# Kernel tuning notes

Measured on AMD Instinct MI355X. Metric: run time of the kernel, lower is better.

The kernel has to match this reference:

```python
import jax, jax.numpy as jnp
import numpy as np
from jax import lax

DIM = 64
HID = int(DIM * 2.67)  # 170, matches torch int(dim*ffn_expansion_factor)
EPS_LN = 1e-5
EPS_NORM = 1e-12


def _conv1x1(x, w, b):
    # x: [B,C,H,W], w: [O,C], b: [O]
    return jnp.einsum('oc,bchw->bohw', w, x) + b[None, :, None, None]


def _dwconv3(x, w, b):
    # depthwise 3x3, w: [C,1,3,3]
    y = lax.conv_general_dilated(x, w, (1, 1), 'SAME',
                                 dimension_numbers=('NCHW', 'OIHW', 'NCHW'),
                                 feature_group_count=x.shape[1])
    return y + b[None, :, None, None]


def _ln_channel(x, w, b):
    # WithBias LayerNorm over channel dim (torch does to_3d then LN over c)
    mu = jnp.mean(x, axis=1, keepdims=True)
    var = jnp.mean((x - mu) ** 2, axis=1, keepdims=True)
    return (x - mu) / jnp.sqrt(var + EPS_LN) * w[None, :, None, None] + b[None, :, None, None]


def _l2norm(x):
    n = jnp.sqrt(jnp.sum(x * x, axis=-1, keepdims=True))
    return x / jnp.maximum(n, EPS_NORM)


def _attn_wxw(x, ln_w, ln_b, qkv_w, qkv_b, dw_w, dw_b, pw, pb, temp):
    m = x
    y = _ln_channel(x, ln_w, ln_b)
    qkv = _dwconv3(_conv1x1(y, qkv_w, qkv_b), dw_w, dw_b)
    q, k, v = jnp.split(qkv, 3, axis=1)
    B, C, H, W = q.shape
    q2 = _l2norm(q.reshape(B, C * H, W))  # 'b c h w -> b (c h) w', normalize over w
    k2 = _l2norm(k.reshape(B, C * H, W))
    attn = jax.nn.softmax(jnp.einsum('bnw,bnu->bwu', q2, k2) * temp[0, 0], axis=-1)  # [B,W,W]
    out = jnp.einsum('bchw,bwu->bchu', v, attn)  # v @ attn with broadcast head dim
    return _conv1x1(out, pw, pb) + m


def _attn_hxh(x, ln_w, ln_b, qkv_w, qkv_b, dw_w, dw_b, pw, pb, temp):
    m = x
    y = _ln_channel(x, ln_w, ln_b)
    qkv = _dwconv3(_conv1x1(y, qkv_w, qkv_b), dw_w, dw_b)
    q, k, v = jnp.split(qkv, 3, axis=1)
    B, C, H, W = q.shape
    q2 = _l2norm(jnp.transpose(q, (0, 2, 1, 3)).reshape(B, H, C * W))  # 'b c h w -> b h (c w)'
    k2 = _l2norm(jnp.transpose(k, (0, 2, 1, 3)).reshape(B, H, C * W))
    attn = jax.nn.softmax(jnp.einsum('bhn,bgn->bhg', q2, k2) * temp[0, 0], axis=-1)  # [B,H,H]
    out = jnp.einsum('bhg,bcgw->bchw', attn, v)  # attn @ v with broadcast head dim
    return _conv1x1(out, pw, pb) + m


def _ffn(x, in_w, in_b, dw_w, dw_b, out_w, out_b):
    y = _dwconv3(_conv1x1(x, in_w, in_b), dw_w, dw_b)
    x1, x2 = jnp.split(y, 2, axis=1)
    return _conv1x1(jax.nn.gelu(x1, approximate=False) * x2, out_w, out_b)


def setup_inputs() -> dict:
    key = jax.random.key(0)
    ks = iter(jax.random.split(key, 32))
    B, C, H, W = 4, DIM, 256, 256
    s = 0.02

    def nrm(shape):
        return jax.random.normal(next(ks), shape, dtype=jnp.float32) * s

    d = {
        'x': jax.random.normal(next(ks), (B, C, H, W), dtype=jnp.float32),
        'zero_map': jnp.ones((B, 1, H, W), dtype=jnp.float32),
    }
    for p in ('w', 'h'):
        d[p + '_ln_w'] = jnp.ones((C,), jnp.float32)
        d[p + '_ln_b'] = jnp.zeros((C,), jnp.float32)
        d[p + '_qkv_w'] = nrm((3 * C, C))
        d[p + '_qkv_b'] = jnp.zeros((3 * C,), jnp.float32)
        d[p + '_dw_w'] = nrm((3 * C, 1, 3, 3))
        d[p + '_dw_b'] = jnp.zeros((3 * C,), jnp.float32)
        d[p + '_proj_w'] = nrm((C, C))
        d[p + '_proj_b'] = jnp.zeros((C,), jnp.float32)
        d[p + '_temp'] = jnp.ones((1, 1), jnp.float32)
    d['n2_w'] = jnp.ones((C,), jnp.float32)
    d['n2_b'] = jnp.zeros((C,), jnp.float32)
    d['ffn_in_w'] = nrm((2 * HID, C))
    d['ffn_in_b'] = jnp.zeros((2 * HID,), jnp.float32)
    d['ffn_dw_w'] = nrm((2 * HID, 1, 3, 3))
    d['ffn_dw_b'] = jnp.zeros((2 * HID,), jnp.float32)
    d['ffn_out_w'] = nrm((C, HID))
    d['ffn_out_b'] = jnp.zeros((C,), jnp.float32)
    return d


def reference(x, zero_map,
              w_ln_w, w_ln_b, w_qkv_w, w_qkv_b, w_dw_w, w_dw_b, w_proj_w, w_proj_b, w_temp,
              h_ln_w, h_ln_b, h_qkv_w, h_qkv_b, h_dw_w, h_dw_b, h_proj_w, h_proj_b, h_temp,
              n2_w, n2_b,
              ffn_in_w, ffn_in_b, ffn_dw_w, ffn_dw_b, ffn_out_w, ffn_out_b):
    # DeepTransformerBlock_withnoZeromap.forward (zero_map is unused in the torch code)
    m = _attn_wxw(x, w_ln_w, w_ln_b, w_qkv_w, w_qkv_b, w_dw_w, w_dw_b, w_proj_w, w_proj_b, w_temp)
    z = _attn_hxh(m, h_ln_w, h_ln_b, h_qkv_w, h_qkv_b, h_dw_w, h_dw_b, h_proj_w, h_proj_b, h_temp)
    return z + _ffn(_ln_channel(z, n2_w, n2_b), ffn_in_w, ffn_in_b, ffn_dw_w, ffn_dw_b, ffn_out_w, ffn_out_b)
```

## Files before the change

kernel.cpp:

```cpp
#include <hip/hip_runtime.h>
#include <math.h>
#include <stdint.h>

#define P_ 65536

#define DW_OFF   0ul
#define QKV_OFF  12582912ul
#define ATTP_OFF QKV_OFF
#define Y_OFF    25165824ul
#define ATT_OFF  31457280ul
#define HID_OFF  0ul
#define G_OFF    22282240ul
#define WSB      33423360ul

typedef unsigned short ush;
typedef __attribute__((ext_vector_type(8))) short bf16x8;
typedef __attribute__((ext_vector_type(4))) float f32x4;

__device__ __forceinline__ ush f2bf(float f) {
    uint32_t u = __float_as_uint(f);
    return (ush)((u + 0x7FFFu + ((u >> 16) & 1u)) >> 16);
}
__device__ __forceinline__ float bf2f(ush h) {
    return __uint_as_float((uint32_t)h << 16);
}

template<int CIN, int CPAD, int COUT, int COPAD, int PX, bool LN, bool RES,
         bool INBF, bool OUTBF>
__global__ __launch_bounds__(256) void conv_mfma_kernel(
        const void* __restrict__ in_, const float* __restrict__ lnw,
        const float* __restrict__ lnb, const float* __restrict__ Wt,
        const float* __restrict__ bias, void* __restrict__ out_,
        const float* __restrict__ res_, size_t zi, size_t zo, size_t zr) {
    static_assert(!(RES && OUTBF), "res only with fp32 out");
    constexpr int NSL = CPAD / 32;
    constexpr int NMT = PX / 16;
    constexpr bool HOIST = (CPAD == 64 && PX == 128);
    __shared__ ush sX[PX * CPAD];
    __shared__ ush sW[COPAD * CPAD];
    __shared__ float sPa[LN ? 256 : 1], sPb[LN ? 256 : 1];
    __shared__ float sMu[LN ? 128 : 1], sInv[LN ? 128 : 1];
    int tid = threadIdx.x;
    int hw0 = blockIdx.x * PX;
    int obase = blockIdx.y * COPAD;
    int lane = tid & 63, wave = tid >> 6;

    {
        uint32_t* sX32 = (uint32_t*)sX;
        #pragma unroll
        for (int it = 0; it < PX * CPAD / 512; ++it) {
            int idx = tid + it * 256;
            int p = idx & (PX - 1), c = (idx / PX) * 2;
            uint32_t pk;
            if constexpr (INBF) {
                const ush* in = (const ush*)in_ + (size_t)blockIdx.z * zi;
                ush a = (c < CIN)     ? in[(size_t)c * P_ + hw0 + p]     : (ush)0;
                ush b = (c + 1 < CIN) ? in[(size_t)(c+1) * P_ + hw0 + p] : (ush)0;
                pk = (uint32_t)a | ((uint32_t)b << 16);
            } else {
                const float* in = (const float*)in_ + (size_t)blockIdx.z * zi;
                float v0 = (c < CIN)     ? in[(size_t)c * P_ + hw0 + p]     : 0.f;
                float v1 = (c + 1 < CIN) ? in[(size_t)(c+1) * P_ + hw0 + p] : 0.f;
                pk = (uint32_t)f2bf(v0) | ((uint32_t)f2bf(v1) << 16);
            }
            int kb = c >> 3;
            sX32[(p * CPAD + (((kb ^ (p & 7)) << 3) | (c & 7))) >> 1] = pk;
        }
    }
    {
        uint32_t* sW32 = (uint32_t*)sW;
        #pragma unroll
        for (int it = 0; it < COPAD * CPAD / 512; ++it) {
            int idx = tid + it * 256;
            int c2 = idx % (CPAD / 2), o = idx / (CPAD / 2);
            int c = c2 * 2, og = obase + o;
            float v0 = (og < COUT && c < CIN)     ? Wt[(size_t)og * CIN + c]     : 0.f;
            float v1 = (og < COUT && c + 1 < CIN) ? Wt[(size_t)og * CIN + c + 1] : 0.f;
            uint32_t pk = (uint32_t)f2bf(v0) | ((uint32_t)f2bf(v1) << 16);
            int kb = c >> 3;
            sW32[(o * CPAD + (((kb ^ (o & 7)) << 3) | (c & 7))) >> 1] = pk;
        }
    }
    __syncthreads();
    if constexpr (LN) {
        static_assert(!LN || (CPAD == 64 && PX == 128), "LN path assumes 64ch/128px");
        int p = tid & 127, q = tid >> 7;
        float s = 0.f, s2 = 0.f;
        #pragma unroll
        for (int c = q * 32; c < q * 32 + 32; ++c) {
            float v = bf2f(sX[p * 64 + ((((c >> 3) ^ (p & 7)) << 3) | (c & 7))]);
            s += v; s2 += v * v;
        }
        sPa[tid] = s; sPb[tid] = s2;
        __syncthreads();
        if (tid < 128) {
            float ss = sPa[tid] + sPa[tid+128];
            float qq = sPb[tid] + sPb[tid+128];
            float mu = ss * (1.f/64.f);
            float var = qq * (1.f/64.f) - mu * mu;
            sMu[tid] = mu; sInv[tid] = rsqrtf(var + 1e-5f);
        }
        __syncthreads();
        float mu = sMu[p], inv = sInv[p];
        #pragma unroll
        for (int c = q * 32; c < q * 32 + 32; ++c) {
            int sw = p * 64 + ((((c >> 3) ^ (p & 7)) << 3) | (c & 7));
            float v = bf2f(sX[sw]);
            sX[sw] = f2bf((v - mu) * inv * lnw[c] + lnb[c]);
        }
        __syncthreads();
    }

    int pxl = lane & 15, quad = lane >> 4;
    int olim = (COUT - obase < COPAD) ? (COUT - obase) : COPAD;
    int ntile = (olim + 15) >> 4;
    bf16x8 xf[HOIST ? NMT * NSL : 1];
    if constexpr (HOIST) {
        #pragma unroll
        for (int m = 0; m < NMT; ++m)
            #pragma unroll
            for (int s = 0; s < NSL; ++s) {
                int p = m * 16 + pxl;
                int kb = s * 4 + quad;
                xf[m * NSL + s] = *(const bf16x8*)&sX[p * CPAD + ((kb ^ (p & 7)) << 3)];
            }
    }
    for (int ot = wave; ot < ntile; ot += 4) {
        int on = ot * 16 + pxl;
        int og = obase + on;
        f32x4 acc[NMT];
        #pragma unroll
        for (int m = 0; m < NMT; ++m) acc[m] = (f32x4){0.f, 0.f, 0.f, 0.f};
        #pragma unroll
        for (int s = 0; s < NSL; ++s) {
            int kb = s * 4 + quad;
            bf16x8 wf = *(const bf16x8*)&sW[on * CPAD + ((kb ^ (on & 7)) << 3)];
            #pragma unroll
            for (int m = 0; m < NMT; ++m) {
                bf16x8 af;
                if constexpr (HOIST) af = xf[m * NSL + s];
                else {
                    int p = m * 16 + pxl;
                    af = *(const bf16x8*)&sX[p * CPAD + ((kb ^ (p & 7)) << 3)];
                }
                acc[m] = __builtin_amdgcn_mfma_f32_16x16x32_bf16(af, wf, acc[m], 0, 0, 0);
            }
        }
        bool oval = og < COUT;
        float bv = oval ? bias[og] : 0.f;
        #pragma unroll
        for (int m = 0; m < NMT; ++m) {
            if (oval) {
                size_t ob = (size_t)og * P_ + hw0 + m * 16 + quad * 4;
                if constexpr (OUTBF) {
                    ush* out = (ush*)out_ + (size_t)blockIdx.z * zo;
                    ushort4 sv;
                    sv.x = f2bf(acc[m][0] + bv); sv.y = f2bf(acc[m][1] + bv);
                    sv.z = f2bf(acc[m][2] + bv); sv.w = f2bf(acc[m][3] + bv);
                    *(ushort4*)&out[ob] = sv;
                } else {
                    float* out = (float*)out_ + (size_t)blockIdx.z * zo;
                    float4 v = make_float4(acc[m][0] + bv, acc[m][1] + bv,
                                           acc[m][2] + bv, acc[m][3] + bv);
                    if constexpr (RES) {
                        const float* res = res_ + (size_t)blockIdx.z * zr;
                        float4 rv = *(const float4*)&res[ob];
                        v.x += rv.x; v.y += rv.y; v.z += rv.z; v.w += rv.w;
                    }
                    *(float4*)&out[ob] = v;
                }
            }
        }
    }
}

__device__ __forceinline__ void mfma_step64(const ush* sA,
        const ush* sB, int wave, int lane, f32x4 acc[2][8]) {
    int pxl = lane & 15, quad = lane >> 4;
    #pragma unroll
    for (int s = 0; s < 2; ++s) {
        int kb = s * 4 + quad;
        bf16x8 af[2];
        #pragma unroll
        for (int mt = 0; mt < 2; ++mt) {
            int im = wave * 32 + mt * 16 + pxl;
            af[mt] = *(const bf16x8*)&sA[im * 64 + ((kb ^ (im & 7)) << 3)];
        }
        #pragma unroll
        for (int jt = 0; jt < 8; ++jt) {
            int jn = jt * 16 + pxl;
            bf16x8 bf = *(const bf16x8*)&sB[jn * 64 + ((kb ^ (jn & 7)) << 3)];
            #pragma unroll
            for (int mt = 0; mt < 2; ++mt)
                acc[mt][jt] = __builtin_amdgcn_mfma_f32_16x16x32_bf16(af[mt], bf, acc[mt][jt], 0, 0, 0);
        }
    }
}

#define STAGE_DIRECT64(sDst, ROWADDR, Q)                                     \
    {   uint32_t* s32_ = (uint32_t*)(sDst);                                  \
        _Pragma("unroll")                                                    \
        for (int it_ = 0; it_ < 8; ++it_) {                                  \
            int idx_ = tid + it_ * 256;                                      \
            int il_ = idx_ >> 4, k_ = (idx_ & 15) * 4;                       \
            float4 v_ = *(const float4*)(ROWADDR(il_) + (Q) * 64 + k_);      \
            uint32_t p0_ = (uint32_t)f2bf(v_.x) | ((uint32_t)f2bf(v_.y) << 16); \
            uint32_t p1_ = (uint32_t)f2bf(v_.z) | ((uint32_t)f2bf(v_.w) << 16); \
            int off_ = il_ * 64 + ((((k_ >> 3) ^ (il_ & 7)) << 3) | (k_ & 7)); \
            s32_[off_ >> 1] = p0_;                                           \
            s32_[(off_ >> 1) + 1] = p1_;                                     \
        }                                                                    \
    }

#define STAGE_TRANS64(sDst, KROWADDR, Q)                                     \
    {   _Pragma("unroll")                                                    \
        for (int it_ = 0; it_ < 8; ++it_) {                                  \
            int idx_ = tid + it_ * 256;                                      \
            int r_ = idx_ >> 5, il4_ = (idx_ & 31) * 4;                      \
            float4 v_ = *(const float4*)(KROWADDR((Q) * 64 + r_) + il4_);    \
            float vv_[4] = {v_.x, v_.y, v_.z, v_.w};                         \
            int kb_ = r_ >> 3;                                               \
            _Pragma("unroll")                                                \
            for (int e_ = 0; e_ < 4; ++e_) {                                 \
                int il_ = il4_ + e_;                                         \
                (sDst)[il_ * 64 + (((kb_ ^ (il_ & 7)) << 3) | (r_ & 7))] = f2bf(vv_[e_]); \
            }                                                                \
        }                                                                    \
    }

#define STAGE_DIRECT64_BF(sDst, ROWADDR, Q)                                  \
    {   _Pragma("unroll")                                                    \
        for (int it_ = 0; it_ < 8; ++it_) {                                  \
            int idx_ = tid + it_ * 256;                                      \
            int il_ = idx_ >> 4, k_ = (idx_ & 15) * 4;                       \
            ushort4 v_ = *(const ushort4*)(ROWADDR(il_) + (Q) * 64 + k_);    \
            int off_ = il_ * 64 + ((((k_ >> 3) ^ (il_ & 7)) << 3) | (k_ & 7)); \
            *(ushort4*)&(sDst)[off_] = v_;                                   \
        }                                                                    \
    }

#define STAGE_TRANS64_BF(sDst, KROWADDR, Q)                                  \
    {   _Pragma("unroll")                                                    \
        for (int it_ = 0; it_ < 8; ++it_) {                                  \
            int idx_ = tid + it_ * 256;                                      \
            int r_ = idx_ >> 5, il4_ = (idx_ & 31) * 4;                      \
            ushort4 v_ = *(const ushort4*)(KROWADDR((Q) * 64 + r_) + il4_);  \
            ush vv_[4] = {v_.x, v_.y, v_.z, v_.w};                          \
            int kb_ = r_ >> 3;                                               \
            _Pragma("unroll")                                                \
            for (int e_ = 0; e_ < 4; ++e_) {                                 \
                int il_ = il4_ + e_;                                         \
                (sDst)[il_ * 64 + (((kb_ ^ (il_ & 7)) << 3) | (r_ & 7))] = vv_[e_]; \
            }                                                                \
        }                                                                    \
    }

template<bool HXH>
__global__ __launch_bounds__(256) void attn_logits_mfma(const ush* __restrict__ dw_,
        float* __restrict__ part_, size_t zd, size_t zp) {
    __shared__ ush sA[128 * 64];
    __shared__ ush sB[128 * 64];
    const ush* dw = dw_ + (size_t)blockIdx.z * zd;
    float* part = part_ + (size_t)blockIdx.z * zp;
    int tid = threadIdx.x, lane = tid & 63, wave = tid >> 6;
    int i0 = (blockIdx.x & 1) * 128, j0 = (blockIdx.x >> 1) * 128;
    int ks = blockIdx.y;
    const ush* qc = dw + ((size_t)ks << 16);
    const ush* kc = dw + ((size_t)(64 + ks) << 16);
    f32x4 acc[2][8];
    #pragma unroll
    for (int mt = 0; mt < 2; ++mt)
        #pragma unroll
        for (int jt = 0; jt < 8; ++jt) acc[mt][jt] = (f32x4){0.f, 0.f, 0.f, 0.f};
    for (int q = 0; q < 4; ++q) {
        if (q) __syncthreads();
        if constexpr (HXH) {
            #define ROWA_Q(il) (qc + (size_t)(i0 + (il)) * 256)
            #define ROWA_K(il) (kc + (size_t)(j0 + (il)) * 256)
            STAGE_DIRECT64_BF(sA, ROWA_Q, q)
            STAGE_DIRECT64_BF(sB, ROWA_K, q)
            #undef ROWA_Q
            #undef ROWA_K
        } else {
            #define KROW_Q(r) (qc + (size_t)(r) * 256 + i0)
            #define KROW_K(r) (kc + (size_t)(r) * 256 + j0)
            STAGE_TRANS64_BF(sA, KROW_Q, q)
            STAGE_TRANS64_BF(sB, KROW_K, q)
            #undef KROW_Q
            #undef KROW_K
        }
        __syncthreads();
        mfma_step64(sA, sB, wave, lane, acc);
    }
    int pxl = lane & 15, quad = lane >> 4;
    float* pb = part + ((size_t)ks << 16);
    #pragma unroll
    for (int mt = 0; mt < 2; ++mt) {
        #pragma unroll
        for (int jt = 0; jt < 8; ++jt) {
            #pragma unroll
            for (int r = 0; r < 4; ++r) {
                int i = i0 + wave * 32 + mt * 16 + quad * 4 + r;
                int j = j0 + jt * 16 + pxl;
                pb[(size_t)i * 256 + j] = acc[mt][jt][r];
            }
        }
    }
}

__global__ __launch_bounds__(256) void av_w_mfma(const ush* __restrict__ dw_,
        const float* __restrict__ att_, ush* __restrict__ out_,
        size_t zd, size_t za, size_t zo) {
    __shared__ ush sA[128 * 64];
    __shared__ ush sB[128 * 64];
    const ush* dw = dw_ + (size_t)blockIdx.z * zd;
    const float* att = att_ + (size_t)blockIdx.z * za;
    ush* out = out_ + (size_t)blockIdx.z * zo;
    int tid = threadIdx.x, lane = tid & 63, wave = tid >> 6;
    int m0 = blockIdx.x * 128, u0 = blockIdx.y * 128;
    f32x4 acc[2][8];
    #pragma unroll
    for (int mt = 0; mt < 2; ++mt)
        #pragma unroll
        for (int jt = 0; jt < 8; ++jt) acc[mt][jt] = (f32x4){0.f, 0.f, 0.f, 0.f};
    for (int q = 0; q < 4; ++q) {
        if (q) __syncthreads();
        #define ROWA_V(il) (dw + ((size_t)(128 + ((m0 + (il)) & 63)) << 16) \
                               + ((m0 + (il)) >> 6) * 256)
        #define KROW_ATT(r) (att + (size_t)(r) * 256 + u0)
        STAGE_DIRECT64_BF(sA, ROWA_V, q)
        STAGE_TRANS64(sB, KROW_ATT, q)
        #undef ROWA_V
        #undef KROW_ATT
        __syncthreads();
        mfma_step64(sA, sB, wave, lane, acc);
    }
    int pxl = lane & 15, quad = lane >> 4;
    #pragma unroll
    for (int mt = 0; mt < 2; ++mt) {
        #pragma unroll
        for (int jt = 0; jt < 8; ++jt) {
            #pragma unroll
            for (int r = 0; r < 4; ++r) {
                int m = m0 + wave * 32 + mt * 16 + quad * 4 + r;
                int c = m & 63, h = m >> 6;
                out[((size_t)c << 16) + h * 256 + u0 + jt * 16 + pxl] = f2bf(acc[mt][jt][r]);
            }
        }
    }
}

__global__ __launch_bounds__(256) void av_h_mfma(const ush* __restrict__ dw_,
        const float* __restrict__ att_, ush* __restrict__ out_,
        size_t zd, size_t za, size_t zo) {
    __shared__ ush sA[128 * 64];
    __shared__ ush sB[128 * 64];
    const ush* dw = dw_ + (size_t)blockIdx.z * zd;
    const float* att = att_ + (size_t)blockIdx.z * za;
    ush* out = out_ + (size_t)blockIdx.z * zo;
    int tid = threadIdx.x, lane = tid & 63, wave = tid >> 6;
    int c = blockIdx.x >> 1;
    int w0 = (blockIdx.x & 1) * 128;
    int h0 = blockIdx.y * 128;
    const ush* vc = dw + ((size_t)(128 + c) << 16);
    f32x4 acc[2][8];
    #pragma unroll
    for (int mt = 0; mt < 2; ++mt)
        #pragma unroll
        for (int jt = 0; jt < 8; ++jt) acc[mt][jt] = (f32x4){0.f, 0.f, 0.f, 0.f};
    for (int q = 0; q < 4; ++q) {
        if (q) __syncthreads();
        #define ROWA_ATT(il) (att + (size_t)(h0 + (il)) * 256)
        #define KROW_V(r) (vc + (size_t)(r) * 256 + w0)
        STAGE_DIRECT64(sA, ROWA_ATT, q)
        STAGE_TRANS64_BF(sB, KROW_V, q)
        #undef ROWA_ATT
        #undef KROW_V
        __syncthreads();
        mfma_step64(sA, sB, wave, lane, acc);
    }
    int pxl = lane & 15, quad = lane >> 4;
    #pragma unroll
    for (int mt = 0; mt < 2; ++mt) {
        #pragma unroll
        for (int jt = 0; jt < 8; ++jt) {
            #pragma unroll
            for (int r = 0; r < 4; ++r) {
                int h = h0 + wave * 32 + mt * 16 + quad * 4 + r;
                out[((size_t)c << 16) + h * 256 + w0 + jt * 16 + pxl] = f2bf(acc[mt][jt][r]);
            }
        }
    }
}

__global__ __launch_bounds__(256) void softmax_kernel(const float* __restrict__ part_,
        const float* __restrict__ temp, float* __restrict__ att_,
        size_t zp, size_t za) {
    const float* part = part_ + (size_t)blockIdx.z * zp;
    float* att = att_ + (size_t)blockIdx.z * za;
    int i = blockIdx.x;
    int j = threadIdx.x;
    size_t rowoff = (size_t)i * 256 + j;
    float s = 0.f;
    #pragma unroll
    for (int kk = 0; kk < 64; ++kk) s += part[(size_t)kk * 65536 + rowoff];
    s *= temp[0];
    __shared__ float redA[4], redB[4];
    int wv = j >> 6, ln = j & 63;
    float m = s;
    #pragma unroll
    for (int off = 32; off; off >>= 1) m = fmaxf(m, __shfl_down(m, off, 64));
    if (ln == 0) redA[wv] = m;
    __syncthreads();
    m = fmaxf(fmaxf(redA[0], redA[1]), fmaxf(redA[2], redA[3]));
    float e = expf(s - m);
    float t2 = e;
    #pragma unroll
    for (int off = 32; off; off >>= 1) t2 += __shfl_down(t2, off, 64);
    if (ln == 0) redB[wv] = t2;
    __syncthreads();
    float tot = redB[0] + redB[1] + redB[2] + redB[3];
    att[rowoff] = e / tot;
}

template<bool NORM>
__global__ __launch_bounds__(256) void dw_row_kernel(const ush* __restrict__ in_,
        const float* __restrict__ w9, const float* __restrict__ bias,
        ush* __restrict__ out_, size_t zi, size_t zo) {
    const ush* in = in_ + (size_t)blockIdx.z * zi;
    ush* out = out_ + (size_t)blockIdx.z * zo;
    int row = __builtin_amdgcn_readfirstlane(blockIdx.x * 4 + (threadIdx.x >> 6));
    int o = row >> 8, h = row & 255;
    int lane = threadIdx.x & 63;
    const ush* ip = in + ((size_t)o << 16);
    const float* wp = w9 + o * 9;
    float b = bias[o];
    float4 acc = make_float4(b, b, b, b);
    #pragma unroll
    for (int dy = -1; dy <= 1; ++dy) {
        int hh = h + dy;
        float4 v = make_float4(0.f, 0.f, 0.f, 0.f);
        if (hh >= 0 && hh <= 255) {
            ushort4 t = *(const ushort4*)(ip + hh * 256 + lane * 4);
            v = make_float4(bf2f(t.x), bf2f(t.y), bf2f(t.z), bf2f(t.w));
        }
        float lft = __shfl(v.w, lane - 1);
        float rgt = __shfl(v.x, lane + 1);
        if (lane == 0)  lft = 0.f;
        if (lane == 63) rgt = 0.f;
        float w0 = wp[(dy+1)*3], w1 = wp[(dy+1)*3+1], w2 = wp[(dy+1)*3+2];
        acc.x += w0*lft + w1*v.x + w2*v.y;
        acc.y += w0*v.x + w1*v.y + w2*v.z;
        acc.z += w0*v.y + w1*v.z + w2*v.w;
        acc.w += w0*v.z + w1*v.w + w2*rgt;
    }
    if constexpr (NORM) {
        if (o < 128) {
            float s = acc.x*acc.x + acc.y*acc.y + acc.z*acc.z + acc.w*acc.w;
            #pragma unroll
            for (int off = 32; off; off >>= 1) s += __shfl_xor(s, off, 64);
            float inv = 1.0f / fmaxf(sqrtf(s), 1e-12f);
            acc.x *= inv; acc.y *= inv; acc.z *= inv; acc.w *= inv;
        }
    }
    ushort4 s4;
    s4.x = f2bf(acc.x); s4.y = f2bf(acc.y); s4.z = f2bf(acc.z); s4.w = f2bf(acc.w);
    *(ushort4*)(out + ((size_t)o << 16) + h * 256 + lane * 4) = s4;
}

__global__ __launch_bounds__(256) void ffn_dw_row_kernel(const ush* __restrict__ hid_,
        const float* __restrict__ w9, const float* __restrict__ bias,
        ush* __restrict__ g_, size_t zi, size_t zo) {
    const ush* hid = hid_ + (size_t)blockIdx.z * zi;
    ush* g = g_ + (size_t)blockIdx.z * zo;
    int row = __builtin_amdgcn_readfirstlane(blockIdx.x * 4 + (threadIdx.x >> 6));
    int i = row >> 8, h = row & 255;
    int lane = threadIdx.x & 63;
    const ush* ip1 = hid + ((size_t)i << 16);
    const ush* ip2 = ip1 + ((size_t)170 << 16);
    const float* wp1 = w9 + i * 9;
    const float* wp2 = w9 + (i + 170) * 9;
    float ba = bias[i], bb = bias[i + 170];
    float4 a = make_float4(ba, ba, ba, ba);
    float4 c = make_float4(bb, bb, bb, bb);
    #pragma unroll
    for (int dy = -1; dy <= 1; ++dy) {
        int hh = h + dy;
        float4 v1 = make_float4(0.f, 0.f, 0.f, 0.f);
        float4 v2 = make_float4(0.f, 0.f, 0.f, 0.f);
        if (hh >= 0 && hh <= 255) {
            ushort4 t1 = *(const ushort4*)(ip1 + hh * 256 + lane * 4);
            ushort4 t2 = *(const ushort4*)(ip2 + hh * 256 + lane * 4);
            v1 = make_float4(bf2f(t1.x), bf2f(t1.y), bf2f(t1.z), bf2f(t1.w));
            v2 = make_float4(bf2f(t2.x), bf2f(t2.y), bf2f(t2.z), bf2f(t2.w));
        }
        float l1 = __shfl(v1.w, lane - 1), r1 = __shfl(v1.x, lane + 1);
        float l2 = __shfl(v2.w, lane - 1), r2 = __shfl(v2.x, lane + 1);
        if (lane == 0)  { l1 = 0.f; l2 = 0.f; }
        if (lane == 63) { r1 = 0.f; r2 = 0.f; }
        float u0 = wp1[(dy+1)*3], u1 = wp1[(dy+1)*3+1], u2 = wp1[(dy+1)*3+2];
        float q0 = wp2[(dy+1)*3], q1 = wp2[(dy+1)*3+1], q2 = wp2[(dy+1)*3+2];
        a.x += u0*l1   + u1*v1.x + u2*v1.y;
        a.y += u0*v1.x + u1*v1.y + u2*v1.z;
        a.z += u0*v1.y + u1*v1.z + u2*v1.w;
        a.w += u0*v1.z + u1*v1.w + u2*r1;
        c.x += q0*l2   + q1*v2.x + q2*v2.y;
        c.y += q0*v2.x + q1*v2.y + q2*v2.z;
        c.z += q0*v2.y + q1*v2.z + q2*v2.w;
        c.w += q0*v2.z + q1*v2.w + q2*r2;
    }
    const float ISQ2 = 0.70710678118654752440f;
    ushort4 s4;
    s4.x = f2bf(0.5f * a.x * (1.0f + erff(a.x * ISQ2)) * c.x);
    s4.y = f2bf(0.5f * a.y * (1.0f + erff(a.y * ISQ2)) * c.y);
    s4.z = f2bf(0.5f * a.z * (1.0f + erff(a.z * ISQ2)) * c.z);
    s4.w = f2bf(0.5f * a.w * (1.0f + erff(a.w * ISQ2)) * c.w);
    *(ushort4*)(g + ((size_t)i << 16) + h * 256 + lane * 4) = s4;
}

__global__ __launch_bounds__(256) void l2norm_h_kernel(ush* __restrict__ dw_,
        size_t zd) {
    ush* dw = dw_ + (size_t)blockIdx.z * zd;
    int h = blockIdx.x, qk = blockIdx.y;
    ush* base = dw + ((size_t)(qk*64) << 16) + h*256;
    int tid = threadIdx.x;
    float s = 0.f;
    for (int idx = tid; idx < 4096; idx += 256) {
        int c = idx >> 6, w4 = (idx & 63) * 4;
        ushort4 t = *(const ushort4*)&base[((size_t)c << 16) + w4];
        float a = bf2f(t.x), b = bf2f(t.y), cc = bf2f(t.z), d = bf2f(t.w);
        s += a*a + b*b + cc*cc + d*d;
    }
    #pragma unroll
    for (int off = 32; off; off >>= 1) s += __shfl_down(s, off, 64);
    __shared__ float red[4];
    int wv = tid >> 6, ln = tid & 63;
    if (ln == 0) red[wv] = s;
    __syncthreads();
    float tot = red[0] + red[1] + red[2] + red[3];
    float inv = 1.0f / fmaxf(sqrtf(tot), 1e-12f);
    for (int idx = tid; idx < 4096; idx += 256) {
        int c = idx >> 6, w4 = (idx & 63) * 4;
        ushort4 t = *(const ushort4*)&base[((size_t)c << 16) + w4];
        ushort4 o;
        o.x = f2bf(bf2f(t.x) * inv); o.y = f2bf(bf2f(t.y) * inv);
        o.z = f2bf(bf2f(t.z) * inv); o.w = f2bf(bf2f(t.w) * inv);
        *(ushort4*)&base[((size_t)c << 16) + w4] = o;
    }
}

extern "C" void kernel_launch(void* const* d_in, const int* in_sizes, int n_in,
                              void* d_out, int out_size, void* d_ws, size_t ws_size,
                              hipStream_t stream) {
    (void)in_sizes; (void)n_in; (void)out_size;
    const float* x = (const float*)d_in[0];
    float* ws  = (float*)d_ws;
    float* out = (float*)d_out;
    const size_t XB = (size_t)64 * P_;
    const size_t WSB2 = 2 * WSB;
    const size_t SLAB_BYTES = WSB * sizeof(float);
    int nb = 1;
    if (ws_size >= 4 * SLAB_BYTES) nb = 4;
    else if (ws_size >= 2 * SLAB_BYTES) nb = 2;

    for (int b0 = 0; b0 < 4; b0 += nb) {
        int zc = (4 - b0 < nb) ? (4 - b0) : nb;
        const float* xb = x + (size_t)b0 * XB;
        float* outb = out + (size_t)b0 * XB;
        ush*   DW   = (ush*)(ws + DW_OFF);
        ush*   QKV  = (ush*)(ws + QKV_OFF);
        float* ATTP = ws + ATTP_OFF;
        ush*   Y    = (ush*)(ws + Y_OFF);
        float* ATT  = ws + ATT_OFF;
        ush*   HID  = (ush*)(ws + HID_OFF);
        ush*   G    = (ush*)(ws + G_OFF);

        conv_mfma_kernel<64,64,192,128,128,true,false,false,true>
            <<<dim3(512,2,zc), 256, 0, stream>>>(
                xb, (const float*)d_in[2], (const float*)d_in[3],
                (const float*)d_in[4], (const float*)d_in[5], QKV, nullptr,
                XB, WSB2, 0);
        dw_row_kernel<true><<<dim3(12288,1,zc), 256, 0, stream>>>(QKV,
                (const float*)d_in[6], (const float*)d_in[7], DW, WSB2, WSB2);
        attn_logits_mfma<false><<<dim3(4,64,zc), 256, 0, stream>>>(DW, ATTP, WSB2, WSB);
        softmax_kernel<<<dim3(256,1,zc), 256, 0, stream>>>(ATTP,
                (const float*)d_in[10], ATT, WSB, WSB);
        av_w_mfma<<<dim3(128,2,zc), 256, 0, stream>>>(DW, ATT, Y, WSB2, WSB, WSB2);
        conv_mfma_kernel<64,64,64,64,128,false,true,true,false>
            <<<dim3(512,1,zc), 256, 0, stream>>>(
                Y, nullptr, nullptr,
                (const float*)d_in[8], (const float*)d_in[9], outb, xb,
                WSB2, XB, XB);

        conv_mfma_kernel<64,64,192,128,128,true,false,false,true>
            <<<dim3(512,2,zc), 256, 0, stream>>>(
                outb, (const float*)d_in[11], (const float*)d_in[12],
                (const float*)d_in[13], (const float*)d_in[14], QKV, nullptr,
                XB, WSB2, 0);
        dw_row_kernel<false><<<dim3(12288,1,zc), 256, 0, stream>>>(QKV,
                (const float*)d_in[15], (const float*)d_in[16], DW, WSB2, WSB2);
        l2norm_h_kernel<<<dim3(256,2,zc), 256, 0, stream>>>(DW, WSB2);
        attn_logits_mfma<true><<<dim3(4,64,zc), 256, 0, stream>>>(DW, ATTP, WSB2, WSB);
        softmax_kernel<<<dim3(256,1,zc), 256, 0, stream>>>(ATTP,
                (const float*)d_in[19], ATT, WSB, WSB);
        av_h_mfma<<<dim3(128,2,zc), 256, 0, stream>>>(DW, ATT, Y, WSB2, WSB, WSB2);
        conv_mfma_kernel<64,64,64,64,128,false,true,true,false>
            <<<dim3(512,1,zc), 256, 0, stream>>>(
                Y, nullptr, nullptr,
                (const float*)d_in[17], (const float*)d_in[18], outb, outb,
                WSB2, XB, XB);

        conv_mfma_kernel<64,64,340,128,128,true,false,false,true>
            <<<dim3(512,3,zc), 256, 0, stream>>>(
                outb, (const float*)d_in[20], (const float*)d_in[21],
                (const float*)d_in[22], (const float*)d_in[23], HID, nullptr,
                XB, WSB2, 0);
        ffn_dw_row_kernel<<<dim3(10880,1,zc), 256, 0, stream>>>(HID,
                (const float*)d_in[24], (const float*)d_in[25], G, WSB2, WSB2);
        conv_mfma_kernel<170,192,64,64,64,false,true,true,false>
            <<<dim3(1024,1,zc), 256, 0, stream>>>(
                G, nullptr, nullptr,
                (const float*)d_in[26], (const float*)d_in[27], outb, outb,
                WSB2, XB, XB);
    }
}
```

Baseline: 1.158 ms.

## Fold LayerNorm into conv epilogue, halve logits partials, two rows per dwconv wave

The LayerNorm-fused 1x1 conv no longer normalizes the staged input tile in shared memory. It folds the LN weight into the conv weights and applies mean, inverse std and a precomputed bias correction per output channel in the epilogue. The attention-logits kernel now accumulates two channel slices per block, which halves the partial buffers the softmax must sum. The depthwise conv kernels compute two output rows per wave so neighbouring input rows are loaded once. The LN fold changes where bf16 rounding happens and adds a serial per-channel dot product of length CIN in every block.

```diff
diff --git a/kernel.cpp b/kernel.cpp
--- a/kernel.cpp
+++ b/kernel.cpp
@@ -33,6 +33,7 @@
         const float* __restrict__ bias, void* __restrict__ out_,
         const float* __restrict__ res_, size_t zi, size_t zo, size_t zr) {
     static_assert(!(RES && OUTBF), "res only with fp32 out");
+    static_assert(!LN || (CPAD == 64 && PX == 128), "LN path assumes 64ch/128px");
     constexpr int NSL = CPAD / 32;
     constexpr int NMT = PX / 16;
     constexpr bool HOIST = (CPAD == 64 && PX == 128);
@@ -40,6 +41,7 @@
     __shared__ ush sW[COPAD * CPAD];
     __shared__ float sPa[LN ? 256 : 1], sPb[LN ? 256 : 1];
     __shared__ float sMu[LN ? 128 : 1], sInv[LN ? 128 : 1];
+    __shared__ float sR[LN ? COPAD : 1], sK[LN ? COPAD : 1];
     int tid = threadIdx.x;
     int hw0 = blockIdx.x * PX;
     int obase = blockIdx.y * COPAD;
@@ -76,6 +78,10 @@
             int c = c2 * 2, og = obase + o;
             float v0 = (og < COUT && c < CIN)     ? Wt[(size_t)og * CIN + c]     : 0.f;
             float v1 = (og < COUT && c + 1 < CIN) ? Wt[(size_t)og * CIN + c + 1] : 0.f;
+            if constexpr (LN) {
+                if (og < COUT && c < CIN)     v0 *= lnw[c];
+                if (og < COUT && c + 1 < CIN) v1 *= lnw[c + 1];
+            }
             uint32_t pk = (uint32_t)f2bf(v0) | ((uint32_t)f2bf(v1) << 16);
             int kb = c >> 3;
             sW32[(o * CPAD + (((kb ^ (o & 7)) << 3) | (c & 7))) >> 1] = pk;
@@ -83,7 +89,6 @@
     }
     __syncthreads();
     if constexpr (LN) {
-        static_assert(!LN || (CPAD == 64 && PX == 128), "LN path assumes 64ch/128px");
         int p = tid & 127, q = tid >> 7;
         float s = 0.f, s2 = 0.f;
         #pragma unroll
@@ -92,6 +97,18 @@
             s += v; s2 += v * v;
         }
         sPa[tid] = s; sPb[tid] = s2;
+        if (tid < COPAD) {
+            int og = obase + tid;
+            float r = 0.f, k = 0.f;
+            if (og < COUT) {
+                #pragma unroll 8
+                for (int c = 0; c < CIN; ++c) {
+                    float w = Wt[(size_t)og * CIN + c];
+                    r += w * lnw[c]; k += w * lnb[c];
+                }
+            }
+            sR[tid] = r; sK[tid] = k;
+        }
         __syncthreads();
         if (tid < 128) {
             float ss = sPa[tid] + sPa[tid+128];
@@ -99,14 +116,6 @@
             float mu = ss * (1.f/64.f);
             float var = qq * (1.f/64.f) - mu * mu;
             sMu[tid] = mu; sInv[tid] = rsqrtf(var + 1e-5f);
-        }
-        __syncthreads();
-        float mu = sMu[p], inv = sInv[p];
-        #pragma unroll
-        for (int c = q * 32; c < q * 32 + 32; ++c) {
-            int sw = p * 64 + ((((c >> 3) ^ (p & 7)) << 3) | (c & 7));
-            float v = bf2f(sX[sw]);
-            sX[sw] = f2bf((v - mu) * inv * lnw[c] + lnb[c]);
         }
         __syncthreads();
     }
@@ -148,20 +157,33 @@
         }
         bool oval = og < COUT;
         float bv = oval ? bias[og] : 0.f;
+        float Rv = 0.f, Kv = 0.f;
+        if constexpr (LN) { Rv = oval ? sR[on] : 0.f; Kv = oval ? sK[on] : 0.f; }
         #pragma unroll
         for (int m = 0; m < NMT; ++m) {
             if (oval) {
                 size_t ob = (size_t)og * P_ + hw0 + m * 16 + quad * 4;
+                float o0, o1, o2, o3;
+                if constexpr (LN) {
+                    int pl = m * 16 + quad * 4;
+                    float4 mu = *(float4*)&sMu[pl];
+                    float4 iv = *(float4*)&sInv[pl];
+                    o0 = iv.x * (acc[m][0] - mu.x * Rv) + Kv + bv;
+                    o1 = iv.y * (acc[m][1] - mu.y * Rv) + Kv + bv;
+                    o2 = iv.z * (acc[m][2] - mu.z * Rv) + Kv + bv;
+                    o3 = iv.w * (acc[m][3] - mu.w * Rv) + Kv + bv;
+                } else {
+                    o0 = acc[m][0] + bv; o1 = acc[m][1] + bv;
+                    o2 = acc[m][2] + bv; o3 = acc[m][3] + bv;
+                }
                 if constexpr (OUTBF) {
                     ush* out = (ush*)out_ + (size_t)blockIdx.z * zo;
                     ushort4 sv;
-                    sv.x = f2bf(acc[m][0] + bv); sv.y = f2bf(acc[m][1] + bv);
-                    sv.z = f2bf(acc[m][2] + bv); sv.w = f2bf(acc[m][3] + bv);
+                    sv.x = f2bf(o0); sv.y = f2bf(o1); sv.z = f2bf(o2); sv.w = f2bf(o3);
                     *(ushort4*)&out[ob] = sv;
                 } else {
                     float* out = (float*)out_ + (size_t)blockIdx.z * zo;
-                    float4 v = make_float4(acc[m][0] + bv, acc[m][1] + bv,
-                                           acc[m][2] + bv, acc[m][3] + bv);
+                    float4 v = make_float4(o0, o1, o2, o3);
                     if constexpr (RES) {
                         const float* res = res_ + (size_t)blockIdx.z * zr;
                         float4 rv = *(const float4*)&res[ob];
@@ -264,36 +286,39 @@
     float* part = part_ + (size_t)blockIdx.z * zp;
     int tid = threadIdx.x, lane = tid & 63, wave = tid >> 6;
     int i0 = (blockIdx.x & 1) * 128, j0 = (blockIdx.x >> 1) * 128;
-    int ks = blockIdx.y;
-    const ush* qc = dw + ((size_t)ks << 16);
-    const ush* kc = dw + ((size_t)(64 + ks) << 16);
+    int ks2 = blockIdx.y;
     f32x4 acc[2][8];
     #pragma unroll
     for (int mt = 0; mt < 2; ++mt)
         #pragma unroll
         for (int jt = 0; jt < 8; ++jt) acc[mt][jt] = (f32x4){0.f, 0.f, 0.f, 0.f};
-    for (int q = 0; q < 4; ++q) {
-        if (q) __syncthreads();
-        if constexpr (HXH) {
-            #define ROWA_Q(il) (qc + (size_t)(i0 + (il)) * 256)
-            #define ROWA_K(il) (kc + (size_t)(j0 + (il)) * 256)
-            STAGE_DIRECT64_BF(sA, ROWA_Q, q)
-            STAGE_DIRECT64_BF(sB, ROWA_K, q)
-            #undef ROWA_Q
-            #undef ROWA_K
-        } else {
-            #define KROW_Q(r) (qc + (size_t)(r) * 256 + i0)
-            #define KROW_K(r) (kc + (size_t)(r) * 256 + j0)
-            STAGE_TRANS64_BF(sA, KROW_Q, q)
-            STAGE_TRANS64_BF(sB, KROW_K, q)
-            #undef KROW_Q
-            #undef KROW_K
-        }
-        __syncthreads();
-        mfma_step64(sA, sB, wave, lane, acc);
+    for (int cc = 0; cc < 2; ++cc) {
+        int ks = ks2 * 2 + cc;
+        const ush* qc = dw + ((size_t)ks << 16);
+        const ush* kc = dw + ((size_t)(64 + ks) << 16);
+        for (int q = 0; q < 4; ++q) {
+            if (cc | q) __syncthreads();
+            if constexpr (HXH) {
+                #define ROWA_Q(il) (qc + (size_t)(i0 + (il)) * 256)
+                #define ROWA_K(il) (kc + (size_t)(j0 + (il)) * 256)
+                STAGE_DIRECT64_BF(sA, ROWA_Q, q)
+                STAGE_DIRECT64_BF(sB, ROWA_K, q)
+                #undef ROWA_Q
+                #undef ROWA_K
+            } else {
+                #define KROW_Q(r) (qc + (size_t)(r) * 256 + i0)
+                #define KROW_K(r) (kc + (size_t)(r) * 256 + j0)
+                STAGE_TRANS64_BF(sA, KROW_Q, q)
+                STAGE_TRANS64_BF(sB, KROW_K, q)
+                #undef KROW_Q
+                #undef KROW_K
+            }
+            __syncthreads();
+            mfma_step64(sA, sB, wave, lane, acc);
+        }
     }
     int pxl = lane & 15, quad = lane >> 4;
-    float* pb = part + ((size_t)ks << 16);
+    float* pb = part + ((size_t)ks2 << 16);
     #pragma unroll
     for (int mt = 0; mt < 2; ++mt) {
         #pragma unroll
@@ -403,7 +428,7 @@
     size_t rowoff = (size_t)i * 256 + j;
     float s = 0.f;
     #pragma unroll
-    for (int kk = 0; kk < 64; ++kk) s += part[(size_t)kk * 65536 + rowoff];
+    for (int kk = 0; kk < 32; ++kk) s += part[(size_t)kk * 65536 + rowoff];
     s *= temp[0];
     __shared__ float redA[4], redB[4];
     int wv = j >> 6, ln = j & 63;
@@ -429,43 +454,63 @@
         ush* __restrict__ out_, size_t zi, size_t zo) {
     const ush* in = in_ + (size_t)blockIdx.z * zi;
     ush* out = out_ + (size_t)blockIdx.z * zo;
-    int row = __builtin_amdgcn_readfirstlane(blockIdx.x * 4 + (threadIdx.x >> 6));
-    int o = row >> 8, h = row & 255;
+    int pr = __builtin_amdgcn_readfirstlane(blockIdx.x * 4 + (threadIdx.x >> 6));
+    int o = pr >> 7, h0 = (pr & 127) * 2;
     int lane = threadIdx.x & 63;
     const ush* ip = in + ((size_t)o << 16);
     const float* wp = w9 + o * 9;
     float b = bias[o];
-    float4 acc = make_float4(b, b, b, b);
-    #pragma unroll
-    for (int dy = -1; dy <= 1; ++dy) {
-        int hh = h + dy;
-        float4 v = make_float4(0.f, 0.f, 0.f, 0.f);
+    float4 r[4];
+    float lft[4], rgt[4];
+    #pragma unroll
+    for (int k = 0; k < 4; ++k) {
+        int hh = h0 - 1 + k;
+        r[k] = make_float4(0.f, 0.f, 0.f, 0.f);
         if (hh >= 0 && hh <= 255) {
             ushort4 t = *(const ushort4*)(ip + hh * 256 + lane * 4);
-            v = make_float4(bf2f(t.x), bf2f(t.y), bf2f(t.z), bf2f(t.w));
-        }
-        float lft = __shfl(v.w, lane - 1);
-        float rgt = __shfl(v.x, lane + 1);
-        if (lane == 0)  lft = 0.f;
-        if (lane == 63) rgt = 0.f;
-        float w0 = wp[(dy+1)*3], w1 = wp[(dy+1)*3+1], w2 = wp[(dy+1)*3+2];
-        acc.x += w0*lft + w1*v.x + w2*v.y;
-        acc.y += w0*v.x + w1*v.y + w2*v.z;
-        acc.z += w0*v.y + w1*v.z + w2*v.w;
-        acc.w += w0*v.z + w1*v.w + w2*rgt;
+            r[k] = make_float4(bf2f(t.x), bf2f(t.y), bf2f(t.z), bf2f(t.w));
+        }
+        lft[k] = __shfl(r[k].w, lane - 1);
+        rgt[k] = __shfl(r[k].x, lane + 1);
+        if (lane == 0)  lft[k] = 0.f;
+        if (lane == 63) rgt[k] = 0.f;
+    }
+    float4 a0 = make_float4(b, b, b, b), a1 = a0;
+    #pragma unroll
+    for (int dy = 0; dy < 3; ++dy) {
+        float w0 = wp[dy*3], w1 = wp[dy*3+1], w2 = wp[dy*3+2];
+        float4 v = r[dy]; float l = lft[dy], rr = rgt[dy];
+        a0.x += w0*l   + w1*v.x + w2*v.y;
+        a0.y += w0*v.x + w1*v.y + w2*v.z;
+        a0.z += w0*v.y + w1*v.z + w2*v.w;
+        a0.w += w0*v.z + w1*v.w + w2*rr;
+        v = r[dy+1]; l = lft[dy+1]; rr = rgt[dy+1];
+        a1.x += w0*l   + w1*v.x + w2*v.y;
+        a1.y += w0*v.x + w1*v.y + w2*v.z;
+        a1.z += w0*v.y + w1*v.z + w2*v.w;
+        a1.w += w0*v.z + w1*v.w + w2*rr;
     }
     if constexpr (NORM) {
         if (o < 128) {
-            float s = acc.x*acc.x + acc.y*acc.y + acc.z*acc.z + acc.w*acc.w;
+            float s0 = a0.x*a0.x + a0.y*a0.y + a0.z*a0.z + a0.w*a0.w;
+            float s1 = a1.x*a1.x + a1.y*a1.y + a1.z*a1.z + a1.w*a1.w;
             #pragma unroll
-            for (int off = 32; off; off >>= 1) s += __shfl_xor(s, off, 64);
-            float inv = 1.0f / fmaxf(sqrtf(s), 1e-12f);
-            acc.x *= inv; acc.y *= inv; acc.z *= inv; acc.w *= inv;
+            for (int off = 32; off; off >>= 1) {
+                s0 += __shfl_xor(s0, off, 64);
+                s1 += __shfl_xor(s1, off, 64);
+            }
+            float i0 = 1.0f / fmaxf(sqrtf(s0), 1e-12f);
+            float i1 = 1.0f / fmaxf(sqrtf(s1), 1e-12f);
+            a0.x *= i0; a0.y *= i0; a0.z *= i0; a0.w *= i0;
+            a1.x *= i1; a1.y *= i1; a1.z *= i1; a1.w *= i1;
         }
     }
     ushort4 s4;
-    s4.x = f2bf(acc.x); s4.y = f2bf(acc.y); s4.z = f2bf(acc.z); s4.w = f2bf(acc.w);
-    *(ushort4*)(out + ((size_t)o << 16) + h * 256 + lane * 4) = s4;
+    ush* ob = out + ((size_t)o << 16) + h0 * 256 + lane * 4;
+    s4.x = f2bf(a0.x); s4.y = f2bf(a0.y); s4.z = f2bf(a0.z); s4.w = f2bf(a0.w);
+    *(ushort4*)ob = s4;
+    s4.x = f2bf(a1.x); s4.y = f2bf(a1.y); s4.z = f2bf(a1.z); s4.w = f2bf(a1.w);
+    *(ushort4*)(ob + 256) = s4;
 }
 
 __global__ __launch_bounds__(256) void ffn_dw_row_kernel(const ush* __restrict__ hid_,
@@ -473,49 +518,72 @@
         ush* __restrict__ g_, size_t zi, size_t zo) {
     const ush* hid = hid_ + (size_t)blockIdx.z * zi;
     ush* g = g_ + (size_t)blockIdx.z * zo;
-    int row = __builtin_amdgcn_readfirstlane(blockIdx.x * 4 + (threadIdx.x >> 6));
-    int i = row >> 8, h = row & 255;
+    int pr = __builtin_amdgcn_readfirstlane(blockIdx.x * 4 + (threadIdx.x >> 6));
+    int i = pr >> 7, h0 = (pr & 127) * 2;
     int lane = threadIdx.x & 63;
     const ush* ip1 = hid + ((size_t)i << 16);
     const ush* ip2 = ip1 + ((size_t)170 << 16);
     const float* wp1 = w9 + i * 9;
     const float* wp2 = w9 + (i + 170) * 9;
     float ba = bias[i], bb = bias[i + 170];
-    float4 a = make_float4(ba, ba, ba, ba);
-    float4 c = make_float4(bb, bb, bb, bb);
-    #pragma unroll
-    for (int dy = -1; dy <= 1; ++dy) {
-        int hh = h + dy;
-        float4 v1 = make_float4(0.f, 0.f, 0.f, 0.f);
-        float4 v2 = make_float4(0.f, 0.f, 0.f, 0.f);
+    float4 r1[4], r2[4];
+    float l1[4], g1[4], l2[4], g2[4];
+    #pragma unroll
+    for (int k = 0; k < 4; ++k) {
+        int hh = h0 - 1 + k;
+        r1[k] = make_float4(0.f, 0.f, 0.f, 0.f);
+        r2[k] = r1[k];
         if (hh >= 0 && hh <= 255) {
             ushort4 t1 = *(const ushort4*)(ip1 + hh * 256 + lane * 4);
             ushort4 t2 = *(const ushort4*)(ip2 + hh * 256 + lane * 4);
-            v1 = make_float4(bf2f(t1.x), bf2f(t1.y), bf2f(t1.z), bf2f(t1.w));
-            v2 = make_float4(bf2f(t2.x), bf2f(t2.y), bf2f(t2.z), bf2f(t2.w));
-        }
-        float l1 = __shfl(v1.w, lane - 1), r1 = __shfl(v1.x, lane + 1);
-        float l2 = __shfl(v2.w, lane - 1), r2 = __shfl(v2.x, lane + 1);
-        if (lane == 0)  { l1 = 0.f; l2 = 0.f; }
-        if (lane == 63) { r1 = 0.f; r2 = 0.f; }
-        float u0 = wp1[(dy+1)*3], u1 = wp1[(dy+1)*3+1], u2 = wp1[(dy+1)*3+2];
-        float q0 = wp2[(dy+1)*3], q1 = wp2[(dy+1)*3+1], q2 = wp2[(dy+1)*3+2];
-        a.x += u0*l1   + u1*v1.x + u2*v1.y;
-        a.y += u0*v1.x + u1*v1.y + u2*v1.z;
-        a.z += u0*v1.y + u1*v1.z + u2*v1.w;
-        a.w += u0*v1.z + u1*v1.w + u2*r1;
-        c.x += q0*l2   + q1*v2.x + q2*v2.y;
-        c.y += q0*v2.x + q1*v2.y + q2*v2.z;
-        c.z += q0*v2.y + q1*v2.z + q2*v2.w;
-        c.w += q0*v2.z + q1*v2.w + q2*r2;
+            r1[k] = make_float4(bf2f(t1.x), bf2f(t1.y), bf2f(t1.z), bf2f(t1.w));
+            r2[k] = make_float4(bf2f(t2.x), bf2f(t2.y), bf2f(t2.z), bf2f(t2.w));
+        }
+        l1[k] = __shfl(r1[k].w, lane - 1); g1[k] = __shfl(r1[k].x, lane + 1);
+        l2[k] = __shfl(r2[k].w, lane - 1); g2[k] = __shfl(r2[k].x, lane + 1);
+        if (lane == 0)  { l1[k] = 0.f; l2[k] = 0.f; }
+        if (lane == 63) { g1[k] = 0.f; g2[k] = 0.f; }
+    }
+    float4 a0 = make_float4(ba, ba, ba, ba), a1 = a0;
+    float4 c0 = make_float4(bb, bb, bb, bb), c1 = c0;
+    #pragma unroll
+    for (int dy = 0; dy < 3; ++dy) {
+        float u0 = wp1[dy*3], u1 = wp1[dy*3+1], u2 = wp1[dy*3+2];
+        float q0 = wp2[dy*3], q1 = wp2[dy*3+1], q2 = wp2[dy*3+2];
+        float4 v = r1[dy]; float l = l1[dy], rr = g1[dy];
+        a0.x += u0*l   + u1*v.x + u2*v.y;
+        a0.y += u0*v.x + u1*v.y + u2*v.z;
+        a0.z += u0*v.y + u1*v.z + u2*v.w;
+        a0.w += u0*v.z + u1*v.w + u2*rr;
+        v = r1[dy+1]; l = l1[dy+1]; rr = g1[dy+1];
+        a1.x += u0*l   + u1*v.x + u2*v.y;
+        a1.y += u0*v.x + u1*v.y + u2*v.z;
+        a1.z += u0*v.y + u1*v.z + u2*v.w;
+        a1.w += u0*v.z + u1*v.w + u2*rr;
+        v = r2[dy]; l = l2[dy]; rr = g2[dy];
+        c0.x += q0*l   + q1*v.x + q2*v.y;
+        c0.y += q0*v.x + q1*v.y + q2*v.z;
+        c0.z += q0*v.y + q1*v.z + q2*v.w;
+        c0.w += q0*v.z + q1*v.w + q2*rr;
+        v = r2[dy+1]; l = l2[dy+1]; rr = g2[dy+1];
+        c1.x += q0*l   + q1*v.x + q2*v.y;
+        c1.y += q0*v.x + q1*v.y + q2*v.z;
+        c1.z += q0*v.y + q1*v.z + q2*v.w;
+        c1.w += q0*v.z + q1*v.w + q2*rr;
     }
     const float ISQ2 = 0.70710678118654752440f;
     ushort4 s4;
-    s4.x = f2bf(0.5f * a.x * (1.0f + erff(a.x * ISQ2)) * c.x);
-    s4.y = f2bf(0.5f * a.y * (1.0f + erff(a.y * ISQ2)) * c.y);
-    s4.z = f2bf(0.5f * a.z * (1.0f + erff(a.z * ISQ2)) * c.z);
-    s4.w = f2bf(0.5f * a.w * (1.0f + erff(a.w * ISQ2)) * c.w);
-    *(ushort4*)(g + ((size_t)i << 16) + h * 256 + lane * 4) = s4;
+    ush* ob = g + ((size_t)i << 16) + h0 * 256 + lane * 4;
+    s4.x = f2bf(0.5f * a0.x * (1.0f + erff(a0.x * ISQ2)) * c0.x);
+    s4.y = f2bf(0.5f * a0.y * (1.0f + erff(a0.y * ISQ2)) * c0.y);
+    s4.z = f2bf(0.5f * a0.z * (1.0f + erff(a0.z * ISQ2)) * c0.z);
+    s4.w = f2bf(0.5f * a0.w * (1.0f + erff(a0.w * ISQ2)) * c0.w);
+    *(ushort4*)ob = s4;
+    s4.x = f2bf(0.5f * a1.x * (1.0f + erff(a1.x * ISQ2)) * c1.x);
+    s4.y = f2bf(0.5f * a1.y * (1.0f + erff(a1.y * ISQ2)) * c1.y);
+    s4.z = f2bf(0.5f * a1.z * (1.0f + erff(a1.z * ISQ2)) * c1.z);
+    s4.w = f2bf(0.5f * a1.w * (1.0f + erff(a1.w * ISQ2)) * c1.w);
+    *(ushort4*)(ob + 256) = s4;
 }
 
 __global__ __launch_bounds__(256) void l2norm_h_kernel(ush* __restrict__ dw_,
@@ -580,9 +648,9 @@
                 xb, (const float*)d_in[2], (const float*)d_in[3],
                 (const float*)d_in[4], (const float*)d_in[5], QKV, nullptr,
                 XB, WSB2, 0);
-        dw_row_kernel<true><<<dim3(12288,1,zc), 256, 0, stream>>>(QKV,
+        dw_row_kernel<true><<<dim3(6144,1,zc), 256, 0, stream>>>(QKV,
                 (const float*)d_in[6], (const float*)d_in[7], DW, WSB2, WSB2);
-        attn_logits_mfma<false><<<dim3(4,64,zc), 256, 0, stream>>>(DW, ATTP, WSB2, WSB);
+        attn_logits_mfma<false><<<dim3(4,32,zc), 256, 0, stream>>>(DW, ATTP, WSB2, WSB);
         softmax_kernel<<<dim3(256,1,zc), 256, 0, stream>>>(ATTP,
                 (const float*)d_in[10], ATT, WSB, WSB);
         av_w_mfma<<<dim3(128,2,zc), 256, 0, stream>>>(DW, ATT, Y, WSB2, WSB, WSB2);
@@ -597,10 +665,10 @@
                 outb, (const float*)d_in[11], (const float*)d_in[12],
                 (const float*)d_in[13], (const float*)d_in[14], QKV, nullptr,
                 XB, WSB2, 0);
-        dw_row_kernel<false><<<dim3(12288,1,zc), 256, 0, stream>>>(QKV,
+        dw_row_kernel<false><<<dim3(6144,1,zc), 256, 0, stream>>>(QKV,
                 (const float*)d_in[15], (const float*)d_in[16], DW, WSB2, WSB2);
         l2norm_h_kernel<<<dim3(256,2,zc), 256, 0, stream>>>(DW, WSB2);
-        attn_logits_mfma<true><<<dim3(4,64,zc), 256, 0, stream>>>(DW, ATTP, WSB2, WSB);
+        attn_logits_mfma<true><<<dim3(4,32,zc), 256, 0, stream>>>(DW, ATTP, WSB2, WSB);
         softmax_kernel<<<dim3(256,1,zc), 256, 0, stream>>>(ATTP,
                 (const float*)d_in[19], ATT, WSB, WSB);
         av_h_mfma<<<dim3(128,2,zc), 256, 0, stream>>>(DW, ATT, Y, WSB2, WSB, WSB2);
@@ -615,7 +683,7 @@
                 outb, (const float*)d_in[20], (const float*)d_in[21],
                 (const float*)d_in[22], (const float*)d_in[23], HID, nullptr,
                 XB, WSB2, 0);
-        ffn_dw_row_kernel<<<dim3(10880,1,zc), 256, 0, stream>>>(HID,
+        ffn_dw_row_kernel<<<dim3(5440,1,zc), 256, 0, stream>>>(HID,
                 (const float*)d_in[24], (const float*)d_in[25], G, WSB2, WSB2);
         conv_mfma_kernel<170,192,64,64,64,false,true,true,false>
             <<<dim3(1024,1,zc), 256, 0, stream>>>(
```

Result: no change. 1.169 ms (+0.9%).
